# Kernel optimization log

Measured on AMD Instinct MI355X. Metric: run time of the kernel, lower is better.

The kernel has to match this reference:

```python
import jax, jax.numpy as jnp
import numpy as np

N_ROIS = 10000
N_CLS = 151          # Visual Genome: 150 object classes + background
NMS_THRESH = 0.3     # filter_det default
SCORE_THRESH = 0.05  # ObjectDetector thresh
MAX_PER_IMG = 64     # ObjectDetector max_per_img
PRE_NMS_TOPN = 6000  # filter_det default
POST_NMS_TOPN = 300  # filter_det default


def setup_inputs() -> dict:
    key = jax.random.key(0)
    k1, k2, k3, k4, k5 = jax.random.split(key, 5)
    # class-probability-like scores (rows sum to 1, like the softmax output fed to filter_det)
    scores = jax.nn.softmax(jax.random.normal(k1, (N_ROIS, N_CLS)) * 2.0, axis=1)
    cx = jax.random.uniform(k2, (N_ROIS, N_CLS)) * 992.0
    cy = jax.random.uniform(k3, (N_ROIS, N_CLS)) * 992.0
    w = 4.0 + jax.random.uniform(k4, (N_ROIS, N_CLS)) * 156.0
    h = 4.0 + jax.random.uniform(k5, (N_ROIS, N_CLS)) * 156.0
    boxes = jnp.clip(jnp.stack([cx - w / 2, cy - h / 2, cx + w / 2, cy + h / 2], axis=-1), 0.0, 1023.0)
    return {"scores": scores.astype(jnp.float32), "boxes": boxes.astype(jnp.float32)}


def _nms_keep(scores_c, boxes_c):
    """apply_nms for one class: fixed-iteration greedy NMS -> bool keep mask [N]."""
    n = scores_c.shape[0]
    # pre_nms_topn: only the top-K scoring boxes are NMS candidates
    kth = jax.lax.top_k(scores_c, PRE_NMS_TOPN)[0][-1]
    active0 = scores_c >= kth
    keep0 = jnp.zeros((n,), dtype=bool)
    areas = (boxes_c[:, 2] - boxes_c[:, 0] + 1.0) * (boxes_c[:, 3] - boxes_c[:, 1] + 1.0)

    def step(carry, _):
        active, keep = carry
        s = jnp.where(active, scores_c, -jnp.inf)
        idx = jnp.argmax(s)
        valid = s[idx] > -jnp.inf  # any candidate left?
        keep = keep.at[idx].set(keep[idx] | valid)
        b = boxes_c[idx]
        ix1 = jnp.maximum(b[0], boxes_c[:, 0])
        iy1 = jnp.maximum(b[1], boxes_c[:, 1])
        ix2 = jnp.minimum(b[2], boxes_c[:, 2])
        iy2 = jnp.minimum(b[3], boxes_c[:, 3])
        inter = jnp.maximum(ix2 - ix1 + 1.0, 0.0) * jnp.maximum(iy2 - iy1 + 1.0, 0.0)
        iou = inter / (areas[idx] + areas - inter)
        # suppress iou > thresh (self box has iou 1, so it is removed too)
        active = active & (iou <= NMS_THRESH)
        return (active, keep), None

    (_, keep), _ = jax.lax.scan(step, (active0, keep0), None, length=POST_NMS_TOPN)
    return keep


def reference(scores, boxes):
    """filter_det: per-class NMS mask + cross-class dedupe + top max_per_img."""
    # per-class NMS, vmapped over the class axis -> keep mask [N, C]
    keep = jax.vmap(_nms_keep, in_axes=(1, 1), out_axes=1)(scores, boxes)
    keep = jax.lax.stop_gradient(keep)  # mask built from .data in the original
    # valid_cls: skip background (col 0) and classes whose best score <= thresh
    col_valid = (jnp.max(scores, axis=0) > SCORE_THRESH).at[0].set(False)
    nms_mask = keep & col_valid[None, :]
    dists_all = jnp.where(nms_mask, scores, 0.0)  # nms_mask * scores
    # nms_filter_duplicates: one label per box (argmax over classes)
    scores_pre = jnp.max(dists_all, axis=1)
    labels_pre = jnp.argmax(dists_all, axis=1)
    # sort descending, threshold, cap at max_per_img (fixed-shape top_k + validity mask)
    s_masked = jnp.where(scores_pre > SCORE_THRESH, scores_pre, -jnp.inf)
    top_v, top_i = jax.lax.top_k(s_masked, MAX_PER_IMG)
    valid = top_v > SCORE_THRESH
    top_scores = jnp.where(valid, top_v, 0.0)
    top_labels = jnp.where(valid, labels_pre[top_i], -1)
    top_inds = jnp.where(valid, top_i, -1)
    return dists_all, top_scores, top_inds, top_labels
```

## Files before the change

### kernel.cpp

```cpp
#include <hip/hip_runtime.h>

typedef unsigned long long u64;
typedef unsigned int u32;

#define N_ROIS   10000
#define N_CLS    151
#define PRE_TOPN 6000
#define POST_TOPN 300
#define MAX_PER  64
#define NMS_TH   0.3f
#define SCORE_TH 0.05f

#define BLOCKA   1024
#define BAND_K   1024
#define BANDCAP  2048
#define CHUNK    512
#define CWORDS   (CHUNK / 32)
#define TROWS    10240

#define SBITS_OFF 0
#define KEYS_OFF  40000
#define SBOX_OFF  56384
#define SIDX_OFF  89152
#define SUPP_OFF  97344
#define KBOX_OFF  130112
#define SMEM_BYTES 134976

__device__ __forceinline__ bool suppresses(float4 a, float4 b)
{
#pragma clang fp contract(off)
    float areaa = (a.z - a.x + 1.f) * (a.w - a.y + 1.f);
    float areab = (b.z - b.x + 1.f) * (b.w - b.y + 1.f);
    float ix1 = fmaxf(a.x, b.x), iy1 = fmaxf(a.y, b.y);
    float ix2 = fminf(a.z, b.z), iy2 = fminf(a.w, b.w);
    float iw = fmaxf(ix2 - ix1 + 1.f, 0.f);
    float ih = fmaxf(iy2 - iy1 + 1.f, 0.f);
    float inter = iw * ih;
    float iou = inter / (areaa + areab - inter);
    return iou > NMS_TH;
}

__global__ __launch_bounds__(BLOCKA)
void nms_kernel(const float* __restrict__ scores,
                const float* __restrict__ scoresT,
                const float* __restrict__ boxes,
                float* __restrict__ dists,
                u64* __restrict__ rowkey,
                int useT)
{
    extern __shared__ __align__(16) char smem[];
    __shared__ int s_cnts[32];
    __shared__ int s_cc;
    __shared__ int s_nk;
    __shared__ u32 s_redu[BLOCKA / 64];
    __shared__ u32 s_alive[CWORDS];
    __shared__ u32 s_rz[CWORDS];
    __shared__ int s_wpre[CWORDS];

    u32*    sbits = (u32*)(smem + SBITS_OFF);
    u64*    keys  = (u64*)(smem + KEYS_OFF);
    float4* sbox  = (float4*)(smem + SBOX_OFF);
    u32*    sidx  = (u32*)(smem + SIDX_OFF);
    u32*    supp  = (u32*)(smem + SUPP_OFF);
    float4* kbox  = (float4*)(smem + KBOX_OFF);

    const int c    = blockIdx.x + 1;
    const int tid  = threadIdx.x;
    const int lane = tid & 63, wid = tid >> 6;

    u32 lmax = 0;
    if (useT) {
        const float* colp = scoresT + (size_t)c * TROWS;
        for (int r = tid; r < N_ROIS; r += BLOCKA) {
            u32 b = __float_as_uint(colp[r]);
            sbits[r] = b;
            lmax = b > lmax ? b : lmax;
        }
    } else {
        for (int r = tid; r < N_ROIS; r += BLOCKA) {
            u32 b = __float_as_uint(scores[(size_t)r * N_CLS + c]);
            sbits[r] = b;
            lmax = b > lmax ? b : lmax;
        }
    }
    for (int off = 32; off; off >>= 1) { u32 o = __shfl_down(lmax, off); lmax = o > lmax ? o : lmax; }
    if (lane == 0) s_redu[wid] = lmax;
    if (tid < 32) s_cnts[tid] = 0;
    __syncthreads();
    if (tid == 0) {
        u32 m = s_redu[0];
        for (int w = 1; w < BLOCKA / 64; ++w) m = s_redu[w] > m ? s_redu[w] : m;
        s_redu[0] = m;
        s_nk = 0;
    }
    __syncthreads();
    if (s_redu[0] <= __float_as_uint(SCORE_TH)) return;

    int slot = 0;
    auto count_ge = [&](u32 mid) -> int {
        int cnt = 0;
        const u64* sb2 = (const u64*)sbits;
        for (int r2 = tid; r2 < N_ROIS / 2; r2 += BLOCKA) {
            u64 two = sb2[r2];
            cnt += ((u32)two >= mid) ? 1 : 0;
            cnt += ((u32)(two >> 32) >= mid) ? 1 : 0;
        }
        for (int off = 32; off; off >>= 1) cnt += __shfl_down(cnt, off);
        if (lane == 0) atomicAdd(&s_cnts[slot & 31], cnt);
        __syncthreads();
        int total = s_cnts[slot & 31];
        if (tid == 0) s_cnts[(slot + 16) & 31] = 0;
        ++slot;
        return total;
    };
    auto bin_search = [&](int target, u32* vOut, int* cntOut) {
        u32 lo = 0, hi = 0x7F800000u; int cntLo = N_ROIS;
        while (hi - lo > 1u) {
            u32 mid = lo + ((hi - lo) >> 1);
            int total = count_ge(mid);
            if (total >= target) { lo = mid; cntLo = total; } else hi = mid;
        }
        *vOut = lo; *cntOut = cntLo;
    };

    u32 Vprev = 0x7F800000u;
    int Cprev = 0;
    u32 Vfloor = 0; int fcnt = 0, haveFloor = 0;
    int knum = 0;

    for (int band = 0; band < 12; ++band) {
        if (knum >= POST_TOPN) break;
        u32 Vlo; int cntAt;
        if (band == 0) {
            bin_search(BAND_K, &Vlo, &cntAt);
        } else {
            if (!haveFloor) { bin_search(PRE_TOPN, &Vfloor, &fcnt); haveFloor = 1; }
            if (Vprev <= Vfloor) break;
            u32 v; int cl;
            bin_search(Cprev + BAND_K, &v, &cl);
            if (v <= Vfloor) { Vlo = Vfloor; cntAt = fcnt; }
            else             { Vlo = v;      cntAt = cl;  }
        }
        if (cntAt - Cprev > BANDCAP) {
            u32 v2 = Vlo + 1;
            if (v2 >= Vprev) break;
            Vlo = v2; cntAt = count_ge(v2);
            if (cntAt - Cprev > BANDCAP) break;
        }
        int Cband = cntAt - Cprev;
        if (Cband <= 0) { Vprev = Vlo; Cprev = cntAt; continue; }

        for (int q = tid; q < BANDCAP; q += BLOCKA) keys[q] = 0;
        if (tid == 0) s_cc = 0;
        __syncthreads();
        for (int r = tid; r < TROWS; r += BLOCKA) {
            bool pred = (r < N_ROIS) && (sbits[r] >= Vlo) && (sbits[r] < Vprev);
            u64 ball = __ballot(pred);
            int bpos = 0, bcnt = __popcll(ball);
            if (lane == 0 && bcnt) bpos = atomicAdd(&s_cc, bcnt);
            bpos = __shfl(bpos, 0);
            if (pred) {
                int pos = bpos + __popcll(ball & ((1ull << lane) - 1ull));
                if (pos < BANDCAP)
                    keys[pos] = ((u64)sbits[r] << 32) | (u64)(0xFFFFFFFFu - (u32)r);
            }
        }
        __syncthreads();
        int C = s_cc; if (C > BANDCAP) C = BANDCAP;

        for (u32 k = 2; k <= BANDCAP; k <<= 1) {
            for (u32 j = k >> 1; j > 0; j >>= 1) {
                __syncthreads();
                for (u32 i = tid; i < BANDCAP; i += BLOCKA) {
                    u32 ixj = i ^ j;
                    if (ixj > i) {
                        u64 a = keys[i], b = keys[ixj];
                        if (((i & k) == 0) ? (a < b) : (a > b)) { keys[i] = b; keys[ixj] = a; }
                    }
                }
            }
        }
        __syncthreads();

        for (int q = tid; q < C; q += BLOCKA) {
            u32 r = 0xFFFFFFFFu - (u32)keys[q];
            sidx[q] = r;
            sbox[q] = *(const float4*)(boxes + ((size_t)r * N_CLS + c) * 4);
        }
        __syncthreads();

        for (int base = 0; base < C && knum < POST_TOPN; base += CHUNK) {
            int chunkN = (C - base) < CHUNK ? (C - base) : CHUNK;
            int knum0 = knum;

            if (tid < CHUNK) {
                bool al = false;
                if (tid < chunkN) {
                    al = true;
                    float4 bq = sbox[base + tid];
                    for (int j = 0; j < knum0; ++j)
                        if (suppresses(kbox[j], bq)) { al = false; break; }
                }
                u64 ball = __ballot(al);
                if (lane == 0) { s_alive[wid * 2] = (u32)ball; s_alive[wid * 2 + 1] = (u32)(ball >> 32); }
            }
            if (tid < CWORDS) s_rz[tid] = 0;
            for (int w = tid; w < CHUNK * CWORDS; w += BLOCKA) supp[w] = 0;
            __syncthreads();

            {
                int q = tid >> 1;
                if (q < chunkN && ((s_alive[q >> 5] >> (q & 31)) & 1u)) {
                    float4 bq = sbox[base + q];
                    for (int p = (tid & 1); p < q; p += 2) {
                        if (!((s_alive[p >> 5] >> (p & 31)) & 1u)) continue;
                        if (suppresses(sbox[base + p], bq)) {
                            atomicOr(&supp[p * CWORDS + (q >> 5)], 1u << (q & 31));
                            atomicOr(&s_rz[p >> 5], 1u << (p & 31));
                        }
                    }
                }
            }
            __syncthreads();

            if (wid == 0) {
                u32 aw  = (lane < CWORDS) ? s_alive[lane] : 0u;
                u32 rzw = (lane < CWORDS) ? s_rz[lane] : 0u;
                const int budget = POST_TOPN - knum0;
                int truncTo = -1;
                while (true) {
                    u32 pz = aw & rzw;
                    u64 bal = __ballot(pz != 0u);
                    if (!bal) break;
                    int pl = __ffsll(bal) - 1;
                    u32 wv = __shfl(pz, pl);
                    int b = __ffs(wv) - 1;
                    int p = (pl << 5) + b;
                    int cb = (lane < pl) ? __popc(aw) : ((lane == pl) ? __popc(aw & ((1u << b) - 1u)) : 0);
                    for (int off = 32; off; off >>= 1) cb += __shfl_down(cb, off);
                    int before = __shfl(cb, 0);
                    if (before >= budget) { truncTo = budget; break; }
                    u32 row = supp[p * CWORDS + (lane & (CWORDS - 1))];
                    if (lane < CWORDS) aw &= ~row;
                    if (lane == pl) { aw |= (1u << b); rzw &= ~(1u << b); }
                    if (before + 1 >= budget) { truncTo = budget; break; }
                }
                if (truncTo < 0) {
                    int pcT = __popc(aw);
                    for (int off = 32; off; off >>= 1) pcT += __shfl_down(pcT, off);
                    if (__shfl(pcT, 0) > budget) truncTo = budget;
                }
                if (truncTo >= 0) {
                    int pcf = __popc(aw);
                    int inc = pcf;
                    for (int off = 1; off < 64; off <<= 1) { int o = __shfl_up(inc, off); if (lane >= off) inc += o; }
                    int ex = inc - pcf;
                    int need = truncTo - ex;
                    if (need <= 0) aw = 0;
                    else if (need < pcf) {
                        while (__popc(aw) > need) aw &= ~(1u << (31 - __clz(aw)));
                    }
                }
                if (lane < CWORDS) s_alive[lane] = aw;
                int pcf2 = __popc(aw);
                int inc2 = pcf2;
                for (int off = 1; off < 64; off <<= 1) { int o = __shfl_up(inc2, off); if (lane >= off) inc2 += o; }
                if (lane < CWORDS) s_wpre[lane] = inc2 - pcf2;
                int totF = __shfl(inc2, CWORDS - 1);
                if (lane == 0) s_nk = knum0 + totF;
            }
            __syncthreads();

            if (tid < CHUNK) {
                int w = tid >> 5, b = tid & 31;
                u32 word = s_alive[w];
                if ((word >> b) & 1u) {
                    int rank = knum0 + s_wpre[w] + __popc(word & ((1u << b) - 1u));
                    int q = base + tid;
                    u32 r = sidx[q];
                    u32 sb = sbits[r];
                    kbox[rank] = sbox[q];
                    dists[(size_t)r * N_CLS + c] = __uint_as_float(sb);
                    atomicMax(rowkey + r, ((u64)sb << 32) | (u64)(0xFFFFFFFFu - (u32)c));
                }
            }
            __syncthreads();
            knum = s_nk;
        }

        Vprev = Vlo; Cprev = cntAt;
    }
}

__global__ __launch_bounds__(BLOCKA)
void transpose_kernel(const float* __restrict__ in, float* __restrict__ outT)
{
    __shared__ float tile[32][33];
    int tx = threadIdx.x & 31, ty = threadIdx.x >> 5;
    int rb = blockIdx.x * 32, cb = blockIdx.y * 32;
    int r = rb + ty, cc = cb + tx;
    tile[ty][tx] = (r < N_ROIS && cc < N_CLS) ? in[(size_t)r * N_CLS + cc] : 0.f;
    __syncthreads();
    int oc = cb + ty, orr = rb + tx;
    if (oc < N_CLS) outT[(size_t)oc * TROWS + orr] = tile[tx][ty];
}

__global__ void zero2_kernel(float* __restrict__ a, int na, u64* __restrict__ b, int nb)
{
    int i = blockIdx.x * blockDim.x + threadIdx.x;
    int stride = gridDim.x * blockDim.x;
    for (int t = i; t < na; t += stride) a[t] = 0.f;
    for (int t = i; t < nb; t += stride) b[t] = 0ull;
}

__global__ __launch_bounds__(1024)
void topk_kernel(const u64* __restrict__ rowkey, float* __restrict__ out)
{
    __shared__ u32 shi[N_ROIS];
    __shared__ int s_cnts[32];
    __shared__ int s_cc;
    __shared__ u64 cand[128];
    const int tid = threadIdx.x, lane = tid & 63;

    if (tid < 32) s_cnts[tid] = 0;
    if (tid == 0) s_cc = 0;
    if (tid < 128) cand[tid] = 0;
    for (int i = tid; i < N_ROIS; i += 1024) {
        u64 rk = rowkey[i];
        u32 hb = (u32)(rk >> 32);
        shi[i] = (__uint_as_float(hb) > SCORE_TH) ? hb : 0u;
    }
    __syncthreads();

    int slot = 0;
    u32 lo = 0, hi = 0x7F800000u;
    while (hi - lo > 1u) {
        u32 mid = lo + ((hi - lo) >> 1);
        int cnt = 0;
        const u64* s2 = (const u64*)shi;
        for (int r2 = tid; r2 < N_ROIS / 2; r2 += 1024) {
            u64 two = s2[r2];
            cnt += ((u32)two >= mid) ? 1 : 0;
            cnt += ((u32)(two >> 32) >= mid) ? 1 : 0;
        }
        for (int off = 32; off; off >>= 1) cnt += __shfl_down(cnt, off);
        if (lane == 0) atomicAdd(&s_cnts[slot & 31], cnt);
        __syncthreads();
        int total = s_cnts[slot & 31];
        if (tid == 0) s_cnts[(slot + 16) & 31] = 0;
        ++slot;
        if (total >= MAX_PER) lo = mid; else hi = mid;
    }
    u32 S = lo ? lo : 1u;

    for (int i = tid; i < TROWS; i += 1024) {
        bool pred = (i < N_ROIS) && (shi[i] >= S);
        u64 ball = __ballot(pred);
        int bpos = 0, bcnt = __popcll(ball);
        if (lane == 0 && bcnt) bpos = atomicAdd(&s_cc, bcnt);
        bpos = __shfl(bpos, 0);
        if (pred) {
            int pos = bpos + __popcll(ball & ((1ull << lane) - 1ull));
            if (pos < 128) cand[pos] = ((u64)shi[i] << 32) | (u64)(0xFFFFFFFFu - (u32)i);
        }
    }
    __syncthreads();
    for (u32 k = 2; k <= 128; k <<= 1) {
        for (u32 j = k >> 1; j > 0; j >>= 1) {
            __syncthreads();
            if (tid < 128) {
                u32 i = tid, ixj = i ^ j;
                if (ixj > i) {
                    u64 a = cand[i], b = cand[ixj];
                    if (((i & k) == 0) ? (a < b) : (a > b)) { cand[i] = b; cand[ixj] = a; }
                }
            }
        }
    }
    __syncthreads();

    float* out_s = out + (size_t)N_ROIS * N_CLS;
    float* out_i = out_s + MAX_PER;
    float* out_l = out_i + MAX_PER;
    if (tid < MAX_PER) {
        u64 kk = cand[tid];
        if (kk == 0) { out_s[tid] = 0.f; out_i[tid] = -1.f; out_l[tid] = -1.f; }
        else {
            u32 r = 0xFFFFFFFFu - (u32)kk;
            out_s[tid] = __uint_as_float((u32)(kk >> 32));
            out_i[tid] = (float)r;
            out_l[tid] = (float)(0xFFFFFFFFu - (u32)rowkey[r]);
        }
    }
}

extern "C" void kernel_launch(void* const* d_in, const int* in_sizes, int n_in,
                              void* d_out, int out_size, void* d_ws, size_t ws_size,
                              hipStream_t stream)
{
    const float* scores = (const float*)d_in[0];
    const float* boxes  = (const float*)d_in[1];
    float* out = (float*)d_out;
    u64* rowkey = (u64*)d_ws;

    size_t needT = 80000 + (size_t)N_CLS * TROWS * sizeof(float);
    int useT = (ws_size >= needT) ? 1 : 0;
    float* scoresT = (float*)((char*)d_ws + 80000);

    (void)hipFuncSetAttribute((const void*)nms_kernel,
                              hipFuncAttributeMaxDynamicSharedMemorySize, SMEM_BYTES);

    zero2_kernel<<<1024, 256, 0, stream>>>(out, out_size, rowkey, N_ROIS);
    if (useT) transpose_kernel<<<dim3(320, 5), BLOCKA, 0, stream>>>(scores, scoresT);
    nms_kernel<<<N_CLS - 1, BLOCKA, SMEM_BYTES, stream>>>(scores, scoresT, boxes, out, rowkey, useT);
    topk_kernel<<<1, 1024, 0, stream>>>(rowkey, out);
}
```

Measured before the change: 281.2 us.

## Replace bitonic band sorts with rank sort and radix-bit threshold search

```diff
diff --git a/kernel.cpp b/kernel.cpp
--- a/kernel.cpp
+++ b/kernel.cpp
@@ -12,19 +12,20 @@
 #define SCORE_TH 0.05f
 
 #define BLOCKA   1024
-#define BAND_K   1024
-#define BANDCAP  2048
-#define CHUNK    512
+#define NWAVES   (BLOCKA / 64)
+#define BANDK    512
+#define BANDCAP  1024
+#define CHUNK    640
 #define CWORDS   (CHUNK / 32)
 #define TROWS    10240
 
-#define SBITS_OFF 0
 #define KEYS_OFF  40000
-#define SBOX_OFF  56384
-#define SIDX_OFF  89152
-#define SUPP_OFF  97344
-#define KBOX_OFF  130112
-#define SMEM_BYTES 134976
+#define RNK_OFF   48192
+#define SBOX_OFF  52288
+#define SIDX_OFF  68672
+#define SUPP_OFF  72768
+#define KBOX_OFF  123968
+#define SMEM_BYTES 128832
 
 __device__ __forceinline__ bool suppresses(float4 a, float4 b)
 {
@@ -50,15 +51,16 @@
 {
     extern __shared__ __align__(16) char smem[];
     __shared__ int s_cnts[32];
-    __shared__ int s_cc;
-    __shared__ int s_nk;
-    __shared__ u32 s_redu[BLOCKA / 64];
-    __shared__ u32 s_alive[CWORDS];
-    __shared__ u32 s_rz[CWORDS];
+    __shared__ int s_cc, s_nk;
+    __shared__ u32 s_redu[NWAVES];
+    __shared__ u32 s_alive[CWORDS], s_rz[CWORDS];
     __shared__ int s_wpre[CWORDS];
-
-    u32*    sbits = (u32*)(smem + SBITS_OFF);
+    __shared__ int s_wofs[NWAVES + 1];
+    __shared__ int s_resume;
+
+    u32*    sbits = (u32*)smem;
     u64*    keys  = (u64*)(smem + KEYS_OFF);
+    u32*    rnk   = (u32*)(smem + RNK_OFF);
     float4* sbox  = (float4*)(smem + SBOX_OFF);
     u32*    sidx  = (u32*)(smem + SIDX_OFF);
     u32*    supp  = (u32*)(smem + SUPP_OFF);
@@ -72,15 +74,11 @@
     if (useT) {
         const float* colp = scoresT + (size_t)c * TROWS;
         for (int r = tid; r < N_ROIS; r += BLOCKA) {
-            u32 b = __float_as_uint(colp[r]);
-            sbits[r] = b;
-            lmax = b > lmax ? b : lmax;
+            u32 b = __float_as_uint(colp[r]); sbits[r] = b; lmax = b > lmax ? b : lmax;
         }
     } else {
         for (int r = tid; r < N_ROIS; r += BLOCKA) {
-            u32 b = __float_as_uint(scores[(size_t)r * N_CLS + c]);
-            sbits[r] = b;
-            lmax = b > lmax ? b : lmax;
+            u32 b = __float_as_uint(scores[(size_t)r * N_CLS + c]); sbits[r] = b; lmax = b > lmax ? b : lmax;
         }
     }
     for (int off = 32; off; off >>= 1) { u32 o = __shfl_down(lmax, off); lmax = o > lmax ? o : lmax; }
@@ -89,103 +87,152 @@
     __syncthreads();
     if (tid == 0) {
         u32 m = s_redu[0];
-        for (int w = 1; w < BLOCKA / 64; ++w) m = s_redu[w] > m ? s_redu[w] : m;
-        s_redu[0] = m;
-        s_nk = 0;
+        for (int w = 1; w < NWAVES; ++w) m = s_redu[w] > m ? s_redu[w] : m;
+        s_redu[0] = m; s_nk = 0;
     }
     __syncthreads();
     if (s_redu[0] <= __float_as_uint(SCORE_TH)) return;
 
     int slot = 0;
-    auto count_ge = [&](u32 mid) -> int {
+    auto count_ge = [&](u32 v) -> int {
         int cnt = 0;
         const u64* sb2 = (const u64*)sbits;
         for (int r2 = tid; r2 < N_ROIS / 2; r2 += BLOCKA) {
             u64 two = sb2[r2];
-            cnt += ((u32)two >= mid) ? 1 : 0;
-            cnt += ((u32)(two >> 32) >= mid) ? 1 : 0;
+            cnt += ((u32)two >= v) ? 1 : 0;
+            cnt += ((u32)(two >> 32) >= v) ? 1 : 0;
         }
         for (int off = 32; off; off >>= 1) cnt += __shfl_down(cnt, off);
-        if (lane == 0) atomicAdd(&s_cnts[slot & 31], cnt);
+        if (lane == 0 && cnt) atomicAdd(&s_cnts[slot & 31], cnt);
         __syncthreads();
         int total = s_cnts[slot & 31];
         if (tid == 0) s_cnts[(slot + 16) & 31] = 0;
         ++slot;
         return total;
     };
-    auto bin_search = [&](int target, u32* vOut, int* cntOut) {
-        u32 lo = 0, hi = 0x7F800000u; int cntLo = N_ROIS;
-        while (hi - lo > 1u) {
-            u32 mid = lo + ((hi - lo) >> 1);
-            int total = count_ge(mid);
-            if (total >= target) { lo = mid; cntLo = total; } else hi = mid;
-        }
-        *vOut = lo; *cntOut = cntLo;
-    };
-
-    u32 Vprev = 0x7F800000u;
-    int Cprev = 0;
-    u32 Vfloor = 0; int fcnt = 0, haveFloor = 0;
-    int knum = 0;
-
-    for (int band = 0; band < 12; ++band) {
-        if (knum >= POST_TOPN) break;
-        u32 Vlo; int cntAt;
-        if (band == 0) {
-            bin_search(BAND_K, &Vlo, &cntAt);
-        } else {
-            if (!haveFloor) { bin_search(PRE_TOPN, &Vfloor, &fcnt); haveFloor = 1; }
-            if (Vprev <= Vfloor) break;
-            u32 v; int cl;
-            bin_search(Cprev + BAND_K, &v, &cl);
-            if (v <= Vfloor) { Vlo = Vfloor; cntAt = fcnt; }
-            else             { Vlo = v;      cntAt = cl;  }
-        }
-        if (cntAt - Cprev > BANDCAP) {
-            u32 v2 = Vlo + 1;
-            if (v2 >= Vprev) break;
-            Vlo = v2; cntAt = count_ge(v2);
-            if (cntAt - Cprev > BANDCAP) break;
-        }
-        int Cband = cntAt - Cprev;
-        if (Cband <= 0) { Vprev = Vlo; Cprev = cntAt; continue; }
-
-        for (int q = tid; q < BANDCAP; q += BLOCKA) keys[q] = 0;
+
+    auto compactRange = [&](u32 vlo, u32 vhiX, int pos0) -> int {
         if (tid == 0) s_cc = 0;
         __syncthreads();
         for (int r = tid; r < TROWS; r += BLOCKA) {
-            bool pred = (r < N_ROIS) && (sbits[r] >= Vlo) && (sbits[r] < Vprev);
+            bool pred = (r < N_ROIS) && (sbits[r] >= vlo) && (sbits[r] < vhiX);
             u64 ball = __ballot(pred);
             int bpos = 0, bcnt = __popcll(ball);
             if (lane == 0 && bcnt) bpos = atomicAdd(&s_cc, bcnt);
             bpos = __shfl(bpos, 0);
             if (pred) {
-                int pos = bpos + __popcll(ball & ((1ull << lane) - 1ull));
+                int pos = pos0 + bpos + (int)__popcll(ball & ((1ull << lane) - 1ull));
                 if (pos < BANDCAP)
                     keys[pos] = ((u64)sbits[r] << 32) | (u64)(0xFFFFFFFFu - (u32)r);
             }
         }
         __syncthreads();
-        int C = s_cc; if (C > BANDCAP) C = BANDCAP;
-
-        for (u32 k = 2; k <= BANDCAP; k <<= 1) {
-            for (u32 j = k >> 1; j > 0; j >>= 1) {
-                __syncthreads();
-                for (u32 i = tid; i < BANDCAP; i += BLOCKA) {
-                    u32 ixj = i ^ j;
-                    if (ixj > i) {
-                        u64 a = keys[i], b = keys[ixj];
-                        if (((i & k) == 0) ? (a < b) : (a > b)) { keys[i] = b; keys[ixj] = a; }
+        return s_cc;
+    };
+
+    auto emitEq = [&](u32 v, int rowStart, int pos0, int capN, int* emittedOut) -> int {
+        int run = 0, resume = N_ROIS;
+        for (int r0 = 0; r0 < N_ROIS; r0 += BLOCKA) {
+            if (r0 + BLOCKA <= rowStart) continue;
+            int r = r0 + tid;
+            bool pred = (r < N_ROIS) && (r >= rowStart) && (sbits[r] == v);
+            u64 ball = __ballot(pred);
+            if (lane == 0) s_wofs[wid] = __popcll(ball);
+            __syncthreads();
+            if (tid == 0) {
+                int acc = 0;
+                for (int w = 0; w < NWAVES; ++w) { int cw = s_wofs[w]; s_wofs[w] = acc; acc += cw; }
+                s_wofs[NWAVES] = acc; s_resume = N_ROIS;
+            }
+            __syncthreads();
+            int tot = s_wofs[NWAVES];
+            if (pred) {
+                int idx = run + s_wofs[wid] + (int)__popcll(ball & ((1ull << lane) - 1ull));
+                if (idx < capN) keys[pos0 + idx] = ((u64)v << 32) | (u64)(0xFFFFFFFFu - (u32)r);
+                else atomicMin(&s_resume, r);
+            }
+            __syncthreads();
+            if (run + tot > capN) {
+                resume = s_resume < (r0 + BLOCKA) ? s_resume : (r0 + BLOCKA);
+                run = capN;
+                break;
+            }
+            run += tot;
+        }
+        *emittedOut = run;
+        return resume;
+    };
+
+    u32 Vhi = 0x80000000u;
+    int procCnt = 0, knum = 0;
+    u32 Vfloor = 0; int eligTotal = 0x7FFFFFFF; bool haveFloor = false;
+    u32 eqV = 0; int eqRow = N_ROIS; bool eqPend = false;
+
+    for (int band = 0; band < 64 && knum < POST_TOPN; ++band) {
+        int C = 0;
+        if (eqPend) {
+            int E; int resume = emitEq(eqV, eqRow, 0, BANDCAP, &E);
+            C = E; procCnt += E;
+            if (resume >= N_ROIS) { eqPend = false; Vhi = eqV; }
+            eqRow = resume;
+            if (C == 0) { if (eqPend) break; else continue; }
+        } else {
+            if (band >= 1) {
+                if (!haveFloor) {
+                    u32 V = 0; int cv = N_ROIS;
+                    for (int b = 30; b >= 0; --b) {
+                        u32 cd = V | (1u << b);
+                        int c2 = count_ge(cd);
+                        if (c2 >= PRE_TOPN) { V = cd; cv = c2; }
                     }
-                }
-            }
-        }
-        __syncthreads();
-
+                    Vfloor = V; eligTotal = cv; haveFloor = true;
+                }
+                if (procCnt >= eligTotal) break;
+            }
+            int target = procCnt + BANDK;
+            int capAbs = procCnt + BANDCAP;
+            u32 V = 0; int cv = N_ROIS;
+            for (int b = 30; b >= 16; --b) {
+                u32 cd = V | (1u << b);
+                int c2 = count_ge(cd);
+                if (c2 >= target) { V = cd; cv = c2; }
+            }
+            for (int b = 15; b >= 0 && cv > capAbs; --b) {
+                u32 cd = V | (1u << b);
+                int c2 = count_ge(cd);
+                if (c2 >= target) { V = cd; cv = c2; }
+            }
+            if (haveFloor && V < Vfloor) { V = Vfloor; cv = eligTotal; }
+            if (cv > capAbs) {
+                int ngt = compactRange(V + 1, Vhi, 0);
+                int E; int resume = emitEq(V, 0, ngt, BANDCAP - ngt, &E);
+                C = ngt + E; procCnt += C;
+                eqV = V; eqRow = resume; eqPend = (resume < N_ROIS);
+                if (!eqPend) Vhi = V;
+            } else {
+                C = compactRange(V, Vhi, 0);
+                procCnt = cv; Vhi = V;
+            }
+            if (C <= 0) continue;
+        }
+
+        for (int q = tid; q < BANDCAP; q += BLOCKA) rnk[q] = 0;
+        __syncthreads();
+        {
+            int q0 = tid >> 1, par = tid & 1;
+            for (int q = q0; q < C; q += BLOCKA / 2) {
+                u64 kq = keys[q]; int partial = 0;
+                for (int p = par; p < C; p += 2) partial += (keys[p] > kq) ? 1 : 0;
+                atomicAdd(&rnk[q], (u32)partial);
+            }
+        }
+        __syncthreads();
         for (int q = tid; q < C; q += BLOCKA) {
-            u32 r = 0xFFFFFFFFu - (u32)keys[q];
-            sidx[q] = r;
-            sbox[q] = *(const float4*)(boxes + ((size_t)r * N_CLS + c) * 4);
+            u64 kq = keys[q];
+            u32 pos = rnk[q];
+            u32 r = 0xFFFFFFFFu - (u32)kq;
+            sidx[pos] = r;
+            sbox[pos] = *(const float4*)(boxes + ((size_t)r * N_CLS + c) * 4);
         }
         __syncthreads();
 
@@ -209,10 +256,11 @@
             __syncthreads();
 
             {
-                int q = tid >> 1;
-                if (q < chunkN && ((s_alive[q >> 5] >> (q & 31)) & 1u)) {
+                int q0 = tid >> 1, par = tid & 1;
+                for (int q = q0; q < chunkN; q += BLOCKA / 2) {
+                    if (!((s_alive[q >> 5] >> (q & 31)) & 1u)) continue;
                     float4 bq = sbox[base + q];
-                    for (int p = (tid & 1); p < q; p += 2) {
+                    for (int p = par; p < q; p += 2) {
                         if (!((s_alive[p >> 5] >> (p & 31)) & 1u)) continue;
                         if (suppresses(sbox[base + p], bq)) {
                             atomicOr(&supp[p * CWORDS + (q >> 5)], 1u << (q & 31));
@@ -240,7 +288,8 @@
                     for (int off = 32; off; off >>= 1) cb += __shfl_down(cb, off);
                     int before = __shfl(cb, 0);
                     if (before >= budget) { truncTo = budget; break; }
-                    u32 row = supp[p * CWORDS + (lane & (CWORDS - 1))];
+                    int widx = (lane < CWORDS) ? lane : 0;
+                    u32 row = supp[p * CWORDS + widx];
                     if (lane < CWORDS) aw &= ~row;
                     if (lane == pl) { aw |= (1u << b); rzw &= ~(1u << b); }
                     if (before + 1 >= budget) { truncTo = budget; break; }
@@ -266,7 +315,7 @@
                 int inc2 = pcf2;
                 for (int off = 1; off < 64; off <<= 1) { int o = __shfl_up(inc2, off); if (lane >= off) inc2 += o; }
                 if (lane < CWORDS) s_wpre[lane] = inc2 - pcf2;
-                int totF = __shfl(inc2, CWORDS - 1);
+                int totF = __shfl(inc2, 63);
                 if (lane == 0) s_nk = knum0 + totF;
             }
             __syncthreads();
@@ -287,45 +336,43 @@
             __syncthreads();
             knum = s_nk;
         }
-
-        Vprev = Vlo; Cprev = cntAt;
     }
 }
 
-__global__ __launch_bounds__(BLOCKA)
-void transpose_kernel(const float* __restrict__ in, float* __restrict__ outT)
+__global__ __launch_bounds__(1024)
+void transpose_zero_kernel(const float* __restrict__ in, float* __restrict__ outT,
+                           float* __restrict__ dists, u64* __restrict__ rowkey, int useT)
 {
     __shared__ float tile[32][33];
-    int tx = threadIdx.x & 31, ty = threadIdx.x >> 5;
-    int rb = blockIdx.x * 32, cb = blockIdx.y * 32;
-    int r = rb + ty, cc = cb + tx;
-    tile[ty][tx] = (r < N_ROIS && cc < N_CLS) ? in[(size_t)r * N_CLS + cc] : 0.f;
-    __syncthreads();
-    int oc = cb + ty, orr = rb + tx;
-    if (oc < N_CLS) outT[(size_t)oc * TROWS + orr] = tile[tx][ty];
+    if (useT) {
+        int tx = threadIdx.x & 31, ty = threadIdx.x >> 5;
+        int rb = blockIdx.x * 32, cb = blockIdx.y * 32;
+        int r = rb + ty, cc = cb + tx;
+        tile[ty][tx] = (r < N_ROIS && cc < N_CLS) ? in[(size_t)r * N_CLS + cc] : 0.f;
+        __syncthreads();
+        int oc = cb + ty, orr = rb + tx;
+        if (oc < N_CLS) outT[(size_t)oc * TROWS + orr] = tile[tx][ty];
+    }
+    int bid = blockIdx.y * gridDim.x + blockIdx.x;
+    int flat = bid * 1024 + threadIdx.x;
+    if (flat < N_ROIS * N_CLS) dists[flat] = 0.f;
+    if (flat < N_ROIS) rowkey[flat] = 0ull;
 }
 
-__global__ void zero2_kernel(float* __restrict__ a, int na, u64* __restrict__ b, int nb)
-{
-    int i = blockIdx.x * blockDim.x + threadIdx.x;
-    int stride = gridDim.x * blockDim.x;
-    for (int t = i; t < na; t += stride) a[t] = 0.f;
-    for (int t = i; t < nb; t += stride) b[t] = 0ull;
-}
-
-__global__ __launch_bounds__(1024)
+__global__ __launch_bounds__(BLOCKA)
 void topk_kernel(const u64* __restrict__ rowkey, float* __restrict__ out)
 {
     __shared__ u32 shi[N_ROIS];
     __shared__ int s_cnts[32];
     __shared__ int s_cc;
-    __shared__ u64 cand[128];
-    const int tid = threadIdx.x, lane = tid & 63;
+    __shared__ u64 cand[192];
+    __shared__ int s_wofs[NWAVES + 1];
+    const int tid = threadIdx.x, lane = tid & 63, wid = tid >> 6;
 
     if (tid < 32) s_cnts[tid] = 0;
     if (tid == 0) s_cc = 0;
-    if (tid < 128) cand[tid] = 0;
-    for (int i = tid; i < N_ROIS; i += 1024) {
+    if (tid < 192) cand[tid] = 0;
+    for (int i = tid; i < N_ROIS; i += BLOCKA) {
         u64 rk = rowkey[i];
         u32 hb = (u32)(rk >> 32);
         shi[i] = (__uint_as_float(hb) > SCORE_TH) ? hb : 0u;
@@ -333,64 +380,111 @@
     __syncthreads();
 
     int slot = 0;
-    u32 lo = 0, hi = 0x7F800000u;
-    while (hi - lo > 1u) {
-        u32 mid = lo + ((hi - lo) >> 1);
+    auto count_ge = [&](u32 v) -> int {
         int cnt = 0;
         const u64* s2 = (const u64*)shi;
-        for (int r2 = tid; r2 < N_ROIS / 2; r2 += 1024) {
+        for (int r2 = tid; r2 < N_ROIS / 2; r2 += BLOCKA) {
             u64 two = s2[r2];
-            cnt += ((u32)two >= mid) ? 1 : 0;
-            cnt += ((u32)(two >> 32) >= mid) ? 1 : 0;
+            cnt += ((u32)two >= v) ? 1 : 0;
+            cnt += ((u32)(two >> 32) >= v) ? 1 : 0;
         }
         for (int off = 32; off; off >>= 1) cnt += __shfl_down(cnt, off);
-        if (lane == 0) atomicAdd(&s_cnts[slot & 31], cnt);
+        if (lane == 0 && cnt) atomicAdd(&s_cnts[slot & 31], cnt);
         __syncthreads();
         int total = s_cnts[slot & 31];
         if (tid == 0) s_cnts[(slot + 16) & 31] = 0;
         ++slot;
-        if (total >= MAX_PER) lo = mid; else hi = mid;
-    }
-    u32 S = lo ? lo : 1u;
-
-    for (int i = tid; i < TROWS; i += 1024) {
-        bool pred = (i < N_ROIS) && (shi[i] >= S);
-        u64 ball = __ballot(pred);
-        int bpos = 0, bcnt = __popcll(ball);
-        if (lane == 0 && bcnt) bpos = atomicAdd(&s_cc, bcnt);
-        bpos = __shfl(bpos, 0);
-        if (pred) {
-            int pos = bpos + __popcll(ball & ((1ull << lane) - 1ull));
-            if (pos < 128) cand[pos] = ((u64)shi[i] << 32) | (u64)(0xFFFFFFFFu - (u32)i);
-        }
-    }
-    __syncthreads();
-    for (u32 k = 2; k <= 128; k <<= 1) {
-        for (u32 j = k >> 1; j > 0; j >>= 1) {
-            __syncthreads();
-            if (tid < 128) {
-                u32 i = tid, ixj = i ^ j;
-                if (ixj > i) {
-                    u64 a = cand[i], b = cand[ixj];
-                    if (((i & k) == 0) ? (a < b) : (a > b)) { cand[i] = b; cand[ixj] = a; }
-                }
-            }
-        }
-    }
-    __syncthreads();
+        return total;
+    };
+
+    const int cap = 128;
+    u32 V = 0; int cv = N_ROIS;
+    for (int b = 30; b >= 16; --b) {
+        u32 cd = V | (1u << b);
+        int c2 = count_ge(cd);
+        if (c2 >= MAX_PER) { V = cd; cv = c2; }
+    }
+    for (int b = 15; b >= 0 && cv > cap; --b) {
+        u32 cd = V | (1u << b);
+        int c2 = count_ge(cd);
+        if (c2 >= MAX_PER) { V = cd; cv = c2; }
+    }
+    if (V == 0) { V = 1; cv = count_ge(1); }
+    int C = 0;
+    if (cv > cap) {
+        if (tid == 0) s_cc = 0;
+        __syncthreads();
+        for (int i = tid; i < TROWS; i += BLOCKA) {
+            bool pred = (i < N_ROIS) && (shi[i] >= V + 1);
+            u64 ball = __ballot(pred);
+            int bpos = 0, bcnt = __popcll(ball);
+            if (lane == 0 && bcnt) bpos = atomicAdd(&s_cc, bcnt);
+            bpos = __shfl(bpos, 0);
+            if (pred) {
+                int pos = bpos + (int)__popcll(ball & ((1ull << lane) - 1ull));
+                if (pos < cap) cand[pos] = ((u64)shi[i] << 32) | (u64)(0xFFFFFFFFu - (u32)i);
+            }
+        }
+        __syncthreads();
+        int ngt = s_cc; if (ngt > cap) ngt = cap;
+        int need = MAX_PER - ngt;
+        int run = 0;
+        for (int r0 = 0; r0 < N_ROIS && run < need; r0 += BLOCKA) {
+            int r = r0 + tid;
+            bool pred = (r < N_ROIS) && (shi[r] == V);
+            u64 ball = __ballot(pred);
+            if (lane == 0) s_wofs[wid] = __popcll(ball);
+            __syncthreads();
+            if (tid == 0) {
+                int acc = 0;
+                for (int w = 0; w < NWAVES; ++w) { int cw = s_wofs[w]; s_wofs[w] = acc; acc += cw; }
+                s_wofs[NWAVES] = acc;
+            }
+            __syncthreads();
+            int tot = s_wofs[NWAVES];
+            if (pred) {
+                int idx = run + s_wofs[wid] + (int)__popcll(ball & ((1ull << lane) - 1ull));
+                if (idx < need) cand[ngt + idx] = ((u64)V << 32) | (u64)(0xFFFFFFFFu - (u32)r);
+            }
+            __syncthreads();
+            run += tot;
+        }
+        C = ngt + (run < need ? run : need);
+    } else {
+        if (tid == 0) s_cc = 0;
+        __syncthreads();
+        for (int i = tid; i < TROWS; i += BLOCKA) {
+            bool pred = (i < N_ROIS) && (shi[i] >= V);
+            u64 ball = __ballot(pred);
+            int bpos = 0, bcnt = __popcll(ball);
+            if (lane == 0 && bcnt) bpos = atomicAdd(&s_cc, bcnt);
+            bpos = __shfl(bpos, 0);
+            if (pred) {
+                int pos = bpos + (int)__popcll(ball & ((1ull << lane) - 1ull));
+                if (pos < cap) cand[pos] = ((u64)shi[i] << 32) | (u64)(0xFFFFFFFFu - (u32)i);
+            }
+        }
+        __syncthreads();
+        C = s_cc; if (C > cap) C = cap;
+    }
 
     float* out_s = out + (size_t)N_ROIS * N_CLS;
     float* out_i = out_s + MAX_PER;
     float* out_l = out_i + MAX_PER;
-    if (tid < MAX_PER) {
-        u64 kk = cand[tid];
-        if (kk == 0) { out_s[tid] = 0.f; out_i[tid] = -1.f; out_l[tid] = -1.f; }
-        else {
-            u32 r = 0xFFFFFFFFu - (u32)kk;
-            out_s[tid] = __uint_as_float((u32)(kk >> 32));
-            out_i[tid] = (float)r;
-            out_l[tid] = (float)(0xFFFFFFFFu - (u32)rowkey[r]);
-        }
+
+    int myrank = -1; u64 myk = 0;
+    if (tid < C) {
+        myk = cand[tid];
+        myrank = 0;
+        for (int p = 0; p < C; ++p) myrank += (cand[p] > myk) ? 1 : 0;
+    }
+    if (tid < MAX_PER) { out_s[tid] = 0.f; out_i[tid] = -1.f; out_l[tid] = -1.f; }
+    __syncthreads();
+    if (tid < C && myrank < MAX_PER) {
+        u32 r = 0xFFFFFFFFu - (u32)myk;
+        out_s[myrank] = __uint_as_float((u32)(myk >> 32));
+        out_i[myrank] = (float)r;
+        out_l[myrank] = (float)(0xFFFFFFFFu - (u32)rowkey[r]);
     }
 }
 
@@ -410,8 +504,7 @@
     (void)hipFuncSetAttribute((const void*)nms_kernel,
                               hipFuncAttributeMaxDynamicSharedMemorySize, SMEM_BYTES);
 
-    zero2_kernel<<<1024, 256, 0, stream>>>(out, out_size, rowkey, N_ROIS);
-    if (useT) transpose_kernel<<<dim3(320, 5), BLOCKA, 0, stream>>>(scores, scoresT);
+    transpose_zero_kernel<<<dim3(320, 5), 1024, 0, stream>>>(scores, scoresT, out, rowkey, useT);
     nms_kernel<<<N_CLS - 1, BLOCKA, SMEM_BYTES, stream>>>(scores, scoresT, boxes, out, rowkey, useT);
-    topk_kernel<<<1, 1024, 0, stream>>>(rowkey, out);
+    topk_kernel<<<1, BLOCKA, 0, stream>>>(rowkey, out);
 }
```

New measurement: 249.4 us. 1.13x faster.
